# Kernel optimization log

Hardware: AMD Instinct MI355X
Metric: run time of the kernel (lower is better)

## Reference

```python
import jax, jax.numpy as jnp
import numpy as np

N_EMBD = 1024
N_HEAD = 16
B, T = 4, 2048

def setup_inputs() -> dict:
    key = jax.random.key(0)
    ks = jax.random.split(key, 5)
    s_attn = 1.0 / np.sqrt(N_EMBD)
    s_proj = 1.0 / np.sqrt(N_EMBD)
    return {
        "x": jax.random.normal(ks[0], (B, T, N_EMBD), dtype=jnp.float32),
        "w_attn": jax.random.uniform(ks[1], (N_EMBD, 3 * N_EMBD), jnp.float32, -s_attn, s_attn),
        "b_attn": jax.random.uniform(ks[2], (3 * N_EMBD,), jnp.float32, -s_attn, s_attn),
        "w_proj": jax.random.uniform(ks[3], (N_EMBD, N_EMBD), jnp.float32, -s_proj, s_proj),
        "b_proj": jax.random.uniform(ks[4], (N_EMBD,), jnp.float32, -s_proj, s_proj),
    }

def reference(x, w_attn, b_attn, w_proj, b_proj):
    Bx, Tx, C = x.shape
    hd = C // N_HEAD  # head dim
    qkv = x @ w_attn + b_attn                       # [B,T,3C]
    q, k, v = jnp.split(qkv, 3, axis=-1)
    # [B,T,C] -> [B,H,T,hd]
    def heads(t):
        return t.reshape(Bx, Tx, N_HEAD, hd).transpose(0, 2, 1, 3)
    q, k, v = heads(q), heads(k), heads(v)
    att = jnp.einsum('bhqd,bhkd->bhqk', q, k) * (1.0 / np.sqrt(hd))
    causal = jnp.tril(jnp.ones((Tx, Tx), dtype=bool))
    att = jnp.where(causal, att, -jnp.inf)
    att = jax.nn.softmax(att, axis=-1)
    y = jnp.einsum('bhqk,bhkd->bhqd', att, v)       # [B,H,T,hd]
    y = y.transpose(0, 2, 1, 3).reshape(Bx, Tx, C)
    return y @ w_proj + b_proj
```

## Files before the change

### kernel.cpp

```cpp
#include <hip/hip_runtime.h>
#include <cstdint>

typedef unsigned short u16;
typedef short s16x8 __attribute__((ext_vector_type(8)));
typedef short s16x4 __attribute__((ext_vector_type(4)));
typedef float f32x4 __attribute__((ext_vector_type(4)));
typedef float f32x16 __attribute__((ext_vector_type(16)));

#define B_   4
#define T_   2048
#define C_   1024
#define H_   16
#define HD_  64
#define M_   8192
#define N3_  3072

#define QSCALE 0.18033688011112042f

__device__ inline u16 f2b(float f) {
  union { float f; uint32_t u; } v; v.f = f;
  uint32_t u = v.u;
  return (u16)((u + 0x7FFFu + ((u >> 16) & 1u)) >> 16);
}

__device__ inline uint32_t cvtpk(float lo, float hi) {
  uint32_t r;
  asm("v_cvt_pk_bf16_f32 %0, %1, %2" : "=v"(r) : "v"(lo), "v"(hi));
  return r;
}

__device__ inline void gload_lds16(const void* g, void* l) {
  __builtin_amdgcn_global_load_lds(
      (const __attribute__((address_space(1))) void*)g,
      (__attribute__((address_space(3))) void*)l, 16, 0, 0);
}

__global__ __launch_bounds__(256) void cvt_f32_bf16(
    const float* __restrict__ in, u16* __restrict__ out, int n) {
  int i = (blockIdx.x * 256 + threadIdx.x) * 8;
  if (i >= n) return;
  float4 a = *(const float4*)(in + i);
  float4 b = *(const float4*)(in + i + 4);
  s16x8 r;
  r[0] = (short)f2b(a.x); r[1] = (short)f2b(a.y);
  r[2] = (short)f2b(a.z); r[3] = (short)f2b(a.w);
  r[4] = (short)f2b(b.x); r[5] = (short)f2b(b.y);
  r[6] = (short)f2b(b.z); r[7] = (short)f2b(b.w);
  *(s16x8*)(out + i) = r;
}

__global__ __launch_bounds__(256) void cvt_transpose(
    const float* __restrict__ W, u16* __restrict__ WT, int K, int N) {
  __shared__ u16 tile[64][65];
  int n0 = blockIdx.x * 64, k0 = blockIdx.y * 64;
  int j = threadIdx.x & 63, i0 = threadIdx.x >> 6;
#pragma unroll
  for (int i = i0; i < 64; i += 4)
    tile[i][j] = f2b(W[(size_t)(k0 + i) * N + n0 + j]);
  __syncthreads();
#pragma unroll
  for (int i = i0; i < 64; i += 4)
    WT[(size_t)(n0 + i) * K + k0 + j] = tile[j][i];
}

template <int MODE>
__global__ __launch_bounds__(256, 4) void gemm_bt(
    const u16* __restrict__ A, const u16* __restrict__ Bt,
    const float* __restrict__ bias, float* __restrict__ outf,
    u16* __restrict__ qo, u16* __restrict__ ko, u16* __restrict__ vo,
    int M, int N, int K) {
  __shared__ u16 As[128 * 64];
  __shared__ u16 Bs[128 * 64];

  int nwg = gridDim.x;
  int bid0 = blockIdx.x;
  int bid = (bid0 & 7) * (nwg >> 3) + (bid0 >> 3);
  int nbn = N >> 7;
  int bm = bid / nbn, bn = bid % nbn;
  int m0 = bm * 128, n0 = bn * 128;
  int tid = threadIdx.x;
  int lane = tid & 63, w = tid >> 6;
  int wm = (w >> 1) * 64, wn = (w & 1) * 64;
  int l15 = lane & 15, g = lane >> 4;

  f32x4 acc[4][4] = {};

  for (int kb = 0; kb < K; kb += 64) {
    __syncthreads();
#pragma unroll
    for (int p = 0; p < 4; ++p) {
      int idx = p * 256 + tid;
      int row = idx >> 3, pc = idx & 7;
      int sc = (pc ^ (row & 7)) * 8;
      gload_lds16(A  + (size_t)(m0 + row) * K + kb + sc, &As[idx * 8]);
      gload_lds16(Bt + (size_t)(n0 + row) * K + kb + sc, &Bs[idx * 8]);
    }
    __syncthreads();

#pragma unroll
    for (int ks = 0; ks < 2; ++ks) {
      int ck = ((g + 4 * ks) ^ (l15 & 7)) * 8;
      s16x8 af[4], bf[4];
#pragma unroll
      for (int mi = 0; mi < 4; ++mi)
        af[mi] = *(const s16x8*)&As[(wm + mi * 16 + l15) * 64 + ck];
#pragma unroll
      for (int ni = 0; ni < 4; ++ni)
        bf[ni] = *(const s16x8*)&Bs[(wn + ni * 16 + l15) * 64 + ck];
#pragma unroll
      for (int mi = 0; mi < 4; ++mi)
#pragma unroll
        for (int ni = 0; ni < 4; ++ni)
          acc[mi][ni] = __builtin_amdgcn_mfma_f32_16x16x32_bf16(
              af[mi], bf[ni], acc[mi][ni], 0, 0, 0);
    }
  }

#pragma unroll
  for (int mi = 0; mi < 4; ++mi)
#pragma unroll
    for (int ni = 0; ni < 4; ++ni) {
      int col = n0 + wn + ni * 16 + l15;
      float bv = bias[col];
      int row0 = m0 + wm + mi * 16 + g * 4;
      if (MODE == 0) {
#pragma unroll
        for (int r = 0; r < 4; ++r)
          outf[(size_t)(row0 + r) * N + col] = acc[mi][ni][r] + bv;
      } else {
        int which = col >> 10, hc = col & 1023;
        int h = hc >> 6, d = hc & 63;
        int b = row0 >> 11, t0 = row0 & 2047;
        if (which == 2) {
          s16x4 pv;
#pragma unroll
          for (int r = 0; r < 4; ++r) pv[r] = (short)f2b(acc[mi][ni][r] + bv);
          *(s16x4*)(vo + ((size_t)((b * 16 + h) * 64 + d)) * 2048 + t0) = pv;
        } else {
          u16* dst = (which == 0) ? qo : ko;
          float sc2 = (which == 0) ? QSCALE : 1.0f;
#pragma unroll
          for (int r = 0; r < 4; ++r)
            dst[(((size_t)(b * 16 + h)) * 2048 + (t0 + r)) * 64 + d] =
                f2b((acc[mi][ni][r] + bv) * sc2);
        }
      }
    }
}

__global__ __launch_bounds__(256, 3) void attn_fwd(
    const u16* __restrict__ Q, const u16* __restrict__ Kg,
    const u16* __restrict__ Vt, u16* __restrict__ Y) {
  __shared__ u16 Ks[64 * 64];
  __shared__ u16 Vs[64 * 64];

  int bid = blockIdx.x;
  int bh = bid & 63;
  int qb = 15 - (bid >> 6);
  int tid = threadIdx.x, lane = tid & 63, w = tid >> 6;
  int l31 = lane & 31, half = lane >> 5;

  const u16* Qh = Q  + (size_t)bh * T_ * HD_;
  const u16* Kh = Kg + (size_t)bh * T_ * HD_;
  const u16* Vh = Vt + (size_t)bh * HD_ * T_;

  int q0 = qb * 128;
  int qw = q0 + w * 32;
  int qrow = qw + l31;

  s16x8 qa[4];
#pragma unroll
  for (int kst = 0; kst < 4; ++kst)
    qa[kst] = *(const s16x8*)(Qh + (size_t)qrow * HD_ + kst * 16 + half * 8);

  f32x16 oacc[2] = {};
  float m = -3.0e30f, l = 0.f;

  int sr = tid >> 3, sc = tid & 7;
  int wswz = (sr & 7) << 4;
  int rswz = (l31 & 7) << 4;
  char* KsB = (char*)Ks;
  char* VsB = (char*)Vs;

  s16x8 kr0 = *(const s16x8*)(Kh + (size_t)sr * HD_ + sc * 8);
  s16x8 kr1 = *(const s16x8*)(Kh + (size_t)(sr + 32) * HD_ + sc * 8);
  s16x8 vr0 = *(const s16x8*)(Vh + (size_t)sr * T_ + sc * 8);
  s16x8 vr1 = *(const s16x8*)(Vh + (size_t)(sr + 32) * T_ + sc * 8);

  int ntile = 2 * qb + 2;
  for (int kt = 0; kt < ntile; ++kt) {
    int kvb = kt * 64;
    __syncthreads();
    *(s16x8*)(KsB + sr * 128 + ((sc * 16) ^ wswz))        = kr0;
    *(s16x8*)(KsB + (sr + 32) * 128 + ((sc * 16) ^ wswz)) = kr1;
    *(s16x8*)(VsB + sr * 128 + ((sc * 16) ^ wswz))        = vr0;
    *(s16x8*)(VsB + (sr + 32) * 128 + ((sc * 16) ^ wswz)) = vr1;
    __syncthreads();

    {
      int kvn = (kt + 1 < ntile) ? (kt + 1) * 64 : 0;
      kr0 = *(const s16x8*)(Kh + (size_t)(kvn + sr) * HD_ + sc * 8);
      kr1 = *(const s16x8*)(Kh + (size_t)(kvn + sr + 32) * HD_ + sc * 8);
      vr0 = *(const s16x8*)(Vh + (size_t)sr * T_ + kvn + sc * 8);
      vr1 = *(const s16x8*)(Vh + (size_t)(sr + 32) * T_ + kvn + sc * 8);
    }

    if (kvb > qw + 31) continue;

    f32x16 s0 = {}, s1 = {};
    __builtin_amdgcn_s_setprio(1);
#pragma unroll
    for (int kst = 0; kst < 4; ++kst) {
      s16x8 kb0 = *(const s16x8*)(KsB +
          (((l31) * 128 + kst * 32 + half * 16) ^ rswz));
      s0 = __builtin_amdgcn_mfma_f32_32x32x16_bf16(kb0, qa[kst], s0, 0, 0, 0);
      s16x8 kb1 = *(const s16x8*)(KsB +
          (((32 + l31) * 128 + kst * 32 + half * 16) ^ rswz));
      s1 = __builtin_amdgcn_mfma_f32_32x32x16_bf16(kb1, qa[kst], s1, 0, 0, 0);
    }
    __builtin_amdgcn_s_setprio(0);

    if (kvb + 63 > qw) {
#pragma unroll
      for (int r = 0; r < 16; ++r) {
        int kv0 = kvb + (r & 3) + 8 * (r >> 2) + 4 * half;
        if (kv0 > qrow) s0[r] = -1e30f;
        if (kv0 + 32 > qrow) s1[r] = -1e30f;
      }
    }

    float a0 = fmaxf(fmaxf(s0[0], s0[1]), fmaxf(s0[2], s0[3]));
    float a1 = fmaxf(fmaxf(s0[4], s0[5]), fmaxf(s0[6], s0[7]));
    float a2 = fmaxf(fmaxf(s0[8], s0[9]), fmaxf(s0[10], s0[11]));
    float a3 = fmaxf(fmaxf(s0[12], s0[13]), fmaxf(s0[14], s0[15]));
    float a4 = fmaxf(fmaxf(s1[0], s1[1]), fmaxf(s1[2], s1[3]));
    float a5 = fmaxf(fmaxf(s1[4], s1[5]), fmaxf(s1[6], s1[7]));
    float a6 = fmaxf(fmaxf(s1[8], s1[9]), fmaxf(s1[10], s1[11]));
    float a7 = fmaxf(fmaxf(s1[12], s1[13]), fmaxf(s1[14], s1[15]));
    float mx = fmaxf(fmaxf(fmaxf(a0, a1), fmaxf(a2, a3)),
                     fmaxf(fmaxf(a4, a5), fmaxf(a6, a7)));
    mx = fmaxf(mx, __shfl_xor(mx, 32, 64));

    if (!__all(mx <= m + 8.0f)) {
      float mn = fmaxf(m, mx);
      float alpha = __builtin_amdgcn_exp2f(m - mn);
      m = mn;
      l *= alpha;
#pragma unroll
      for (int i = 0; i < 16; ++i) { oacc[0][i] *= alpha; oacc[1][i] *= alpha; }
    }

    float rs = 0.f;
#pragma unroll
    for (int r = 0; r < 16; ++r) {
      float p0 = __builtin_amdgcn_exp2f(s0[r] - m);
      float p1 = __builtin_amdgcn_exp2f(s1[r] - m);
      s0[r] = p0; s1[r] = p1;
      rs += p0 + p1;
    }
    rs += __shfl_xor(rs, 32, 64);
    l += rs;

    s16x8 pb[4];
#pragma unroll
    for (int ks4 = 0; ks4 < 4; ++ks4) {
      const f32x16& sv = (ks4 < 2) ? s0 : s1;
      const int R = (ks4 & 1) * 8;
      uint32_t A0 = cvtpk(sv[R + 0], sv[R + 1]);
      uint32_t A1 = cvtpk(sv[R + 2], sv[R + 3]);
      uint32_t B0 = cvtpk(sv[R + 4], sv[R + 5]);
      uint32_t B1 = cvtpk(sv[R + 6], sv[R + 7]);
      uint32_t r0 = (uint32_t)__shfl_xor((int)(half ? A0 : B0), 32, 64);
      uint32_t r1 = (uint32_t)__shfl_xor((int)(half ? A1 : B1), 32, 64);
      union { uint32_t u[4]; s16x8 v; } pk_;
      pk_.u[0] = half ? r0 : A0;
      pk_.u[1] = half ? r1 : A1;
      pk_.u[2] = half ? B0 : r0;
      pk_.u[3] = half ? B1 : r1;
      pb[ks4] = pk_.v;
    }

    __builtin_amdgcn_s_setprio(1);
#pragma unroll
    for (int hb = 0; hb < 2; ++hb)
#pragma unroll
      for (int ks4 = 0; ks4 < 4; ++ks4) {
        s16x8 va = *(const s16x8*)(VsB +
            (((hb * 32 + l31) * 128 + ks4 * 32 + half * 16) ^ rswz));
        oacc[hb] = __builtin_amdgcn_mfma_f32_32x32x16_bf16(va, pb[ks4],
                                                           oacc[hb], 0, 0, 0);
      }
    __builtin_amdgcn_s_setprio(0);
  }

  int b = bh >> 4, h = bh & 15;
  float inv = 1.0f / l;
  u16* yrow = Y + ((size_t)b * T_ + qrow) * C_ + h * 64;
#pragma unroll
  for (int hb = 0; hb < 2; ++hb)
#pragma unroll
    for (int rg = 0; rg < 4; ++rg) {
      union { uint32_t u[2]; s16x4 v; } o;
      o.u[0] = cvtpk(oacc[hb][rg * 4 + 0] * inv, oacc[hb][rg * 4 + 1] * inv);
      o.u[1] = cvtpk(oacc[hb][rg * 4 + 2] * inv, oacc[hb][rg * 4 + 3] * inv);
      *(s16x4*)(yrow + hb * 32 + rg * 8 + half * 4) = o.v;
    }
}

extern "C" void kernel_launch(void* const* d_in, const int* in_sizes, int n_in,
                              void* d_out, int out_size, void* d_ws, size_t ws_size,
                              hipStream_t stream) {
  const float* x      = (const float*)d_in[0];
  const float* w_attn = (const float*)d_in[1];
  const float* b_attn = (const float*)d_in[2];
  const float* w_proj = (const float*)d_in[3];
  const float* b_proj = (const float*)d_in[4];
  float* out = (float*)d_out;

  u16* ws  = (u16*)d_ws;
  u16* xb  = ws;
  u16* wat = xb  + (size_t)M_ * C_;
  u16* wpt = wat + (size_t)N3_ * C_;
  u16* q   = wpt + (size_t)C_ * C_;
  u16* k   = q   + (size_t)M_ * C_;
  u16* v   = k   + (size_t)M_ * C_;
  u16* ya  = xb;

  cvt_f32_bf16<<<dim3((M_ * C_) / (256 * 8)), dim3(256), 0, stream>>>(x, xb, M_ * C_);
  cvt_transpose<<<dim3(N3_ / 64, C_ / 64), dim3(256), 0, stream>>>(w_attn, wat, C_, N3_);
  cvt_transpose<<<dim3(C_ / 64, C_ / 64), dim3(256), 0, stream>>>(w_proj, wpt, C_, C_);

  gemm_bt<1><<<dim3((M_ / 128) * (N3_ / 128)), dim3(256), 0, stream>>>(
      xb, wat, b_attn, nullptr, q, k, v, M_, N3_, C_);

  attn_fwd<<<dim3(64 * 16), dim3(256), 0, stream>>>(q, k, v, ya);

  gemm_bt<0><<<dim3((M_ / 128) * (C_ / 128)), dim3(256), 0, stream>>>(
      ya, wpt, b_proj, out, nullptr, nullptr, nullptr, M_, C_, C_);
}
```

Measured before the change: 166.5 us.

## Add 256x256 eight-wave ping-pong GEMM for QKV projection

Introduces a new gemm8p kernel with 256x256 tiles, 512 threads and double-buffered LDS. It interleaves global-to-LDS staging with MFMA quadrants under explicit barriers, waitcnts and setprio, and uses it for the QKV projection in place of the 128x128 gemm_bt. The aim is more data reuse per tile and better overlap of memory loads with matrix math. In exchange it uses 128KB of LDS per block and relies on hand-placed synchronization that is fragile and could stall if the waitcnt counts are wrong.

```diff
diff --git a/kernel.cpp b/kernel.cpp
--- a/kernel.cpp
+++ b/kernel.cpp
@@ -61,6 +61,160 @@
 #pragma unroll
   for (int i = i0; i < 64; i += 4)
     WT[(size_t)(n0 + i) * K + k0 + j] = tile[j][i];
+}
+
+template <int MODE>
+__global__ __launch_bounds__(512, 2) void gemm8p(
+    const u16* __restrict__ A, const u16* __restrict__ Bt,
+    const float* __restrict__ bias, float* __restrict__ outf,
+    u16* __restrict__ qo, u16* __restrict__ ko, u16* __restrict__ vo,
+    int M, int N, int K) {
+  __shared__ u16 As[2][2][128 * 64];
+  __shared__ u16 Bs[2][2][128 * 64];
+
+  int nwg = gridDim.x;
+  int bid0 = blockIdx.x;
+  int bid = (bid0 & 7) * (nwg >> 3) + (bid0 >> 3);
+  int nbn = N >> 8;
+  int bm = bid / nbn, bn = bid % nbn;
+  int m0 = bm * 256, n0 = bn * 256;
+  int tid = threadIdx.x, lane = tid & 63, w = tid >> 6;
+  int l15 = lane & 15, g = lane >> 4;
+  int Ah = w >> 2;
+  int Bh = (w & 3) >> 1;
+  int bno = (w & 1) * 64;
+  int nt = K >> 6;
+  int ck0 = (g ^ (l15 & 7)) * 8;
+  int ck1 = ((4 + g) ^ (l15 & 7)) * 8;
+
+  f32x4 acc[8][4] = {};
+  s16x8 af[4][2], bf0[2][2], bf1[2][2];
+
+#define BAR() asm volatile("s_barrier" ::: "memory")
+#define WAITL0() do { asm volatile("s_waitcnt lgkmcnt(0)" ::: "memory"); \
+  __builtin_amdgcn_sched_barrier(0); } while (0)
+#define STAGE_A8(bb, uh, kt) do { \
+  _Pragma("unroll") for (int ld = 0; ld < 2; ++ld) { \
+    int slot = ld * 512 + tid, row = slot >> 3, pc = slot & 7; \
+    int sc = (pc ^ (row & 7)) * 8; \
+    gload_lds16(A + (size_t)(m0 + (uh) * 128 + row) * K + (kt) * 64 + sc, \
+                &As[bb][uh][slot * 8]); \
+  } } while (0)
+#define STAGE_B8(bb, uh, kt) do { \
+  _Pragma("unroll") for (int ld = 0; ld < 2; ++ld) { \
+    int slot = ld * 512 + tid, row = slot >> 3, pc = slot & 7; \
+    int sc = (pc ^ (row & 7)) * 8; \
+    gload_lds16(Bt + (size_t)(n0 + (uh) * 128 + row) * K + (kt) * 64 + sc, \
+                &Bs[bb][uh][slot * 8]); \
+  } } while (0)
+#define LDA8(bb, mq) do { \
+  _Pragma("unroll") for (int mi = 0; mi < 4; ++mi) { \
+    int rw = ((mq) * 64 + mi * 16 + l15) * 64; \
+    af[mi][0] = *(const s16x8*)&As[bb][Ah][rw + ck0]; \
+    af[mi][1] = *(const s16x8*)&As[bb][Ah][rw + ck1]; \
+  } } while (0)
+#define LDB8(bb, nq, bfr) do { \
+  _Pragma("unroll") for (int ni = 0; ni < 2; ++ni) { \
+    int rw = (bno + (nq) * 32 + ni * 16 + l15) * 64; \
+    bfr[ni][0] = *(const s16x8*)&Bs[bb][Bh][rw + ck0]; \
+    bfr[ni][1] = *(const s16x8*)&Bs[bb][Bh][rw + ck1]; \
+  } } while (0)
+#define QUAD8(mq, nq, bfr) do { \
+  __builtin_amdgcn_s_setprio(1); \
+  _Pragma("unroll") for (int mi = 0; mi < 4; ++mi) \
+  _Pragma("unroll") for (int ni = 0; ni < 2; ++ni) \
+  _Pragma("unroll") for (int ks = 0; ks < 2; ++ks) \
+    acc[(mq) * 4 + mi][(nq) * 2 + ni] = \
+        __builtin_amdgcn_mfma_f32_16x16x32_bf16( \
+            af[mi][ks], bfr[ni][ks], acc[(mq) * 4 + mi][(nq) * 2 + ni], \
+            0, 0, 0); \
+  __builtin_amdgcn_s_setprio(0); \
+} while (0)
+
+  STAGE_B8(0, 0, 0); STAGE_B8(0, 1, 0);
+  STAGE_A8(0, 0, 0); STAGE_A8(0, 1, 0);
+  STAGE_B8(1, 0, 1); STAGE_B8(1, 1, 1);
+  asm volatile("s_waitcnt vmcnt(4)" ::: "memory");
+  BAR();
+
+  for (int t = 0; t < nt; t += 2) {
+    int t1 = t + 1;
+    int t2 = (t + 2 < nt) ? t + 2 : 0;
+    int t3 = (t + 3 < nt) ? t + 3 : 1;
+    LDA8(0, 0); LDB8(0, 0, bf0);
+    STAGE_A8(1, 0, t1);
+    asm volatile("s_waitcnt lgkmcnt(8)" ::: "memory");
+    BAR(); WAITL0();
+    QUAD8(0, 0, bf0); BAR();
+    LDB8(0, 1, bf1);
+    STAGE_A8(1, 1, t1);
+    BAR(); WAITL0();
+    QUAD8(0, 1, bf1); BAR();
+    LDA8(0, 1);
+    STAGE_B8(0, 0, t2);
+    BAR(); WAITL0();
+    QUAD8(1, 1, bf1); BAR();
+    STAGE_B8(0, 1, t2);
+    asm volatile("s_waitcnt vmcnt(4)" ::: "memory");
+    BAR();
+    QUAD8(1, 0, bf0); BAR();
+    LDA8(1, 0); LDB8(1, 0, bf0);
+    STAGE_A8(0, 0, t2);
+    asm volatile("s_waitcnt lgkmcnt(8)" ::: "memory");
+    BAR(); WAITL0();
+    QUAD8(0, 0, bf0); BAR();
+    LDB8(1, 1, bf1);
+    STAGE_A8(0, 1, t2);
+    BAR(); WAITL0();
+    QUAD8(0, 1, bf1); BAR();
+    LDA8(1, 1);
+    STAGE_B8(1, 0, t3);
+    BAR(); WAITL0();
+    QUAD8(1, 1, bf1); BAR();
+    STAGE_B8(1, 1, t3);
+    asm volatile("s_waitcnt vmcnt(4)" ::: "memory");
+    BAR();
+    QUAD8(1, 0, bf0); BAR();
+  }
+#undef BAR
+#undef WAITL0
+#undef STAGE_A8
+#undef STAGE_B8
+#undef LDA8
+#undef LDB8
+#undef QUAD8
+
+  int which = (MODE == 1) ? (n0 >> 10) : 0;
+#pragma unroll
+  for (int mf = 0; mf < 8; ++mf)
+#pragma unroll
+    for (int na = 0; na < 4; ++na) {
+      int col = n0 + (w & 3) * 64 + na * 16 + l15;
+      float bv = bias[col];
+      int row0 = m0 + (w >> 2) * 128 + mf * 16 + g * 4;
+      if (MODE == 0) {
+#pragma unroll
+        for (int r = 0; r < 4; ++r)
+          outf[(size_t)(row0 + r) * N + col] = acc[mf][na][r] + bv;
+      } else {
+        int hc = col & 1023;
+        int h = hc >> 6, d = hc & 63;
+        int b = row0 >> 11, t0 = row0 & 2047;
+        if (which == 2) {
+          s16x4 pv;
+#pragma unroll
+          for (int r = 0; r < 4; ++r) pv[r] = (short)f2b(acc[mf][na][r] + bv);
+          *(s16x4*)(vo + ((size_t)((b * 16 + h) * 64 + d)) * 2048 + t0) = pv;
+        } else {
+          u16* dst = (which == 0) ? qo : ko;
+          float sc2 = (which == 0) ? QSCALE : 1.0f;
+#pragma unroll
+          for (int r = 0; r < 4; ++r)
+            dst[(((size_t)(b * 16 + h)) * 2048 + (t0 + r)) * 64 + d] =
+                f2b((acc[mf][na][r] + bv) * sc2);
+        }
+      }
+    }
 }
 
 template <int MODE>
@@ -330,7 +484,7 @@
   cvt_transpose<<<dim3(N3_ / 64, C_ / 64), dim3(256), 0, stream>>>(w_attn, wat, C_, N3_);
   cvt_transpose<<<dim3(C_ / 64, C_ / 64), dim3(256), 0, stream>>>(w_proj, wpt, C_, C_);
 
-  gemm_bt<1><<<dim3((M_ / 128) * (N3_ / 128)), dim3(256), 0, stream>>>(
+  gemm8p<1><<<dim3((M_ / 256) * (N3_ / 256)), dim3(512), 0, stream>>>(
       xb, wat, b_attn, nullptr, q, k, v, M_, N3_, C_);
 
   attn_fwd<<<dim3(64 * 16), dim3(256), 0, stream>>>(q, k, v, ya);
```

New measurement: 173.0 us. 1.04x slower.

## Fuse fp32-to-bf16 conversion of x into QKV GEMM A-tile loading

Applied to the files above, without the earlier changes.

Removes the separate kernel that converted x to bf16. The QKV GEMM now reads fp32 A tiles straight into registers, one k-block ahead, and converts them with v_cvt_pk_bf16_f32 before writing them to LDS with the same swizzle. This drops one kernel launch and a full write plus re-read of the bf16 copy of x. In exchange, each QKV block moves twice as many A bytes (fp32) and is re-read across the 24 column tiles. It also uses more registers and replaces async LDS loads for A with synchronous register staging.

```diff
diff --git a/kernel.cpp b/kernel.cpp
--- a/kernel.cpp
+++ b/kernel.cpp
@@ -35,20 +35,6 @@
       (__attribute__((address_space(3))) void*)l, 16, 0, 0);
 }
 
-__global__ __launch_bounds__(256) void cvt_f32_bf16(
-    const float* __restrict__ in, u16* __restrict__ out, int n) {
-  int i = (blockIdx.x * 256 + threadIdx.x) * 8;
-  if (i >= n) return;
-  float4 a = *(const float4*)(in + i);
-  float4 b = *(const float4*)(in + i + 4);
-  s16x8 r;
-  r[0] = (short)f2b(a.x); r[1] = (short)f2b(a.y);
-  r[2] = (short)f2b(a.z); r[3] = (short)f2b(a.w);
-  r[4] = (short)f2b(b.x); r[5] = (short)f2b(b.y);
-  r[6] = (short)f2b(b.z); r[7] = (short)f2b(b.w);
-  *(s16x8*)(out + i) = r;
-}
-
 __global__ __launch_bounds__(256) void cvt_transpose(
     const float* __restrict__ W, u16* __restrict__ WT, int K, int N) {
   __shared__ u16 tile[64][65];
@@ -63,14 +49,16 @@
     WT[(size_t)(n0 + i) * K + k0 + j] = tile[j][i];
 }
 
-template <int MODE>
+template <int MODE, int AF32>
 __global__ __launch_bounds__(256, 4) void gemm_bt(
-    const u16* __restrict__ A, const u16* __restrict__ Bt,
+    const void* __restrict__ Araw, const u16* __restrict__ Bt,
     const float* __restrict__ bias, float* __restrict__ outf,
     u16* __restrict__ qo, u16* __restrict__ ko, u16* __restrict__ vo,
     int M, int N, int K) {
   __shared__ u16 As[128 * 64];
   __shared__ u16 Bs[128 * 64];
+  const u16*   A16 = (const u16*)Araw;
+  const float* A32 = (const float*)Araw;
 
   int nwg = gridDim.x;
   int bid0 = blockIdx.x;
@@ -85,17 +73,52 @@
 
   f32x4 acc[4][4] = {};
 
+  int tr = tid >> 4;
+  int tc = tid & 15;
+  const float* Afp = AF32 ? (A32 + (size_t)(m0 + tr) * K + tc * 4) : nullptr;
+  int aslot = ((tc >> 1) ^ (tr & 7)) * 8 + (tid & 1) * 4;
+  f32x4 fa[8];
+  if (AF32) {
+#pragma unroll
+    for (int p = 0; p < 8; ++p)
+      fa[p] = *(const f32x4*)(Afp + (size_t)p * 16 * K);
+  }
+
   for (int kb = 0; kb < K; kb += 64) {
     __syncthreads();
-#pragma unroll
-    for (int p = 0; p < 4; ++p) {
-      int idx = p * 256 + tid;
-      int row = idx >> 3, pc = idx & 7;
-      int sc = (pc ^ (row & 7)) * 8;
-      gload_lds16(A  + (size_t)(m0 + row) * K + kb + sc, &As[idx * 8]);
-      gload_lds16(Bt + (size_t)(n0 + row) * K + kb + sc, &Bs[idx * 8]);
+    if (AF32) {
+#pragma unroll
+      for (int p = 0; p < 8; ++p) {
+        uint32_t d0 = cvtpk(fa[p][0], fa[p][1]);
+        uint32_t d1 = cvtpk(fa[p][2], fa[p][3]);
+        uint2 dw; dw.x = d0; dw.y = d1;
+        *(uint2*)&As[(p * 16 + tr) * 64 + aslot] = dw;
+      }
+#pragma unroll
+      for (int p = 0; p < 4; ++p) {
+        int idx = p * 256 + tid;
+        int row = idx >> 3, pc = idx & 7;
+        int sc = (pc ^ (row & 7)) * 8;
+        gload_lds16(Bt + (size_t)(n0 + row) * K + kb + sc, &Bs[idx * 8]);
+      }
+    } else {
+#pragma unroll
+      for (int p = 0; p < 4; ++p) {
+        int idx = p * 256 + tid;
+        int row = idx >> 3, pc = idx & 7;
+        int sc = (pc ^ (row & 7)) * 8;
+        gload_lds16(A16 + (size_t)(m0 + row) * K + kb + sc, &As[idx * 8]);
+        gload_lds16(Bt  + (size_t)(n0 + row) * K + kb + sc, &Bs[idx * 8]);
+      }
     }
     __syncthreads();
+
+    if (AF32) {
+      int kn = (kb + 64 < K) ? kb + 64 : 0;
+#pragma unroll
+      for (int p = 0; p < 8; ++p)
+        fa[p] = *(const f32x4*)(Afp + (size_t)p * 16 * K + kn);
+    }
 
 #pragma unroll
     for (int ks = 0; ks < 2; ++ks) {
@@ -318,23 +341,21 @@
   float* out = (float*)d_out;
 
   u16* ws  = (u16*)d_ws;
-  u16* xb  = ws;
-  u16* wat = xb  + (size_t)M_ * C_;
+  u16* ya  = ws;
+  u16* wat = ya  + (size_t)M_ * C_;
   u16* wpt = wat + (size_t)N3_ * C_;
   u16* q   = wpt + (size_t)C_ * C_;
   u16* k   = q   + (size_t)M_ * C_;
   u16* v   = k   + (size_t)M_ * C_;
-  u16* ya  = xb;
-
-  cvt_f32_bf16<<<dim3((M_ * C_) / (256 * 8)), dim3(256), 0, stream>>>(x, xb, M_ * C_);
+
   cvt_transpose<<<dim3(N3_ / 64, C_ / 64), dim3(256), 0, stream>>>(w_attn, wat, C_, N3_);
   cvt_transpose<<<dim3(C_ / 64, C_ / 64), dim3(256), 0, stream>>>(w_proj, wpt, C_, C_);
 
-  gemm_bt<1><<<dim3((M_ / 128) * (N3_ / 128)), dim3(256), 0, stream>>>(
-      xb, wat, b_attn, nullptr, q, k, v, M_, N3_, C_);
+  gemm_bt<1, 1><<<dim3((M_ / 128) * (N3_ / 128)), dim3(256), 0, stream>>>(
+      x, wat, b_attn, nullptr, q, k, v, M_, N3_, C_);
 
   attn_fwd<<<dim3(64 * 16), dim3(256), 0, stream>>>(q, k, v, ya);
 
-  gemm_bt<0><<<dim3((M_ / 128) * (C_ / 128)), dim3(256), 0, stream>>>(
+  gemm_bt<0, 0><<<dim3((M_ / 128) * (C_ / 128)), dim3(256), 0, stream>>>(
       ya, wpt, b_proj, out, nullptr, nullptr, nullptr, M_, C_, C_);
 }
```

After: 165.6 us. Within noise of the previous version (-0.5%).

## Double per-warp query rows in attention to reuse K/V tiles across two blocks

Applied to the files above, without the earlier changes.

Each warp now processes two 32-row query blocks (256 queries per workgroup instead of 128), so every K/V fragment read from LDS feeds two MFMAs, and each K/V tile is loaded once per 256 queries. The grid halves to 512 workgroups and launch bounds drop to 2 waves-per-SIMD occupancy to fit the doubled accumulators and score registers. The trade-off is lower occupancy, coarser causal-block granularity with more masked waste, and fewer workgroups to balance across CUs.

```diff
diff --git a/kernel.cpp b/kernel.cpp
--- a/kernel.cpp
+++ b/kernel.cpp
@@ -148,7 +148,7 @@
     }
 }
 
-__global__ __launch_bounds__(256, 3) void attn_fwd(
+__global__ __launch_bounds__(256, 2) void attn_fwd(
     const u16* __restrict__ Q, const u16* __restrict__ Kg,
     const u16* __restrict__ Vt, u16* __restrict__ Y) {
   __shared__ u16 Ks[64 * 64];
@@ -156,7 +156,7 @@
 
   int bid = blockIdx.x;
   int bh = bid & 63;
-  int qb = 15 - (bid >> 6);
+  int qb = 7 - (bid >> 6);
   int tid = threadIdx.x, lane = tid & 63, w = tid >> 6;
   int l31 = lane & 31, half = lane >> 5;
 
@@ -164,17 +164,20 @@
   const u16* Kh = Kg + (size_t)bh * T_ * HD_;
   const u16* Vh = Vt + (size_t)bh * HD_ * T_;
 
-  int q0 = qb * 128;
-  int qw = q0 + w * 32;
-  int qrow = qw + l31;
-
-  s16x8 qa[4];
-#pragma unroll
-  for (int kst = 0; kst < 4; ++kst)
-    qa[kst] = *(const s16x8*)(Qh + (size_t)qrow * HD_ + kst * 16 + half * 8);
-
-  f32x16 oacc[2] = {};
-  float m = -3.0e30f, l = 0.f;
+  int q0 = qb * 256;
+  int qw = q0 + w * 64;
+  int qrA = qw + l31;
+  int qrB = qw + 32 + l31;
+
+  s16x8 qaA[4], qaB[4];
+#pragma unroll
+  for (int kst = 0; kst < 4; ++kst) {
+    qaA[kst] = *(const s16x8*)(Qh + (size_t)qrA * HD_ + kst * 16 + half * 8);
+    qaB[kst] = *(const s16x8*)(Qh + (size_t)qrB * HD_ + kst * 16 + half * 8);
+  }
+
+  f32x16 oA0 = {}, oA1 = {}, oB0 = {}, oB1 = {};
+  float mA = -3.0e30f, lA = 0.f, mB = -3.0e30f, lB = 0.f;
 
   int sr = tid >> 3, sc = tid & 7;
   int wswz = (sr & 7) << 4;
@@ -187,7 +190,7 @@
   s16x8 vr0 = *(const s16x8*)(Vh + (size_t)sr * T_ + sc * 8);
   s16x8 vr1 = *(const s16x8*)(Vh + (size_t)(sr + 32) * T_ + sc * 8);
 
-  int ntile = 2 * qb + 2;
+  int ntile = 4 * qb + 4;
   for (int kt = 0; kt < ntile; ++kt) {
     int kvb = kt * 64;
     __syncthreads();
@@ -205,18 +208,20 @@
       vr1 = *(const s16x8*)(Vh + (size_t)(sr + 32) * T_ + kvn + sc * 8);
     }
 
-    if (kvb > qw + 31) continue;
-
-    f32x16 s0 = {}, s1 = {};
+    if (kvb > qw + 63) continue;
+
+    f32x16 sA0 = {}, sA1 = {}, sB0 = {}, sB1 = {};
     __builtin_amdgcn_s_setprio(1);
 #pragma unroll
     for (int kst = 0; kst < 4; ++kst) {
       s16x8 kb0 = *(const s16x8*)(KsB +
-          (((l31) * 128 + kst * 32 + half * 16) ^ rswz));
-      s0 = __builtin_amdgcn_mfma_f32_32x32x16_bf16(kb0, qa[kst], s0, 0, 0, 0);
+          ((l31 * 128 + kst * 32 + half * 16) ^ rswz));
+      sA0 = __builtin_amdgcn_mfma_f32_32x32x16_bf16(kb0, qaA[kst], sA0, 0, 0, 0);
+      sB0 = __builtin_amdgcn_mfma_f32_32x32x16_bf16(kb0, qaB[kst], sB0, 0, 0, 0);
       s16x8 kb1 = *(const s16x8*)(KsB +
           (((32 + l31) * 128 + kst * 32 + half * 16) ^ rswz));
-      s1 = __builtin_amdgcn_mfma_f32_32x32x16_bf16(kb1, qa[kst], s1, 0, 0, 0);
+      sA1 = __builtin_amdgcn_mfma_f32_32x32x16_bf16(kb1, qaA[kst], sA1, 0, 0, 0);
+      sB1 = __builtin_amdgcn_mfma_f32_32x32x16_bf16(kb1, qaB[kst], sB1, 0, 0, 0);
     }
     __builtin_amdgcn_s_setprio(0);
 
@@ -224,87 +229,133 @@
 #pragma unroll
       for (int r = 0; r < 16; ++r) {
         int kv0 = kvb + (r & 3) + 8 * (r >> 2) + 4 * half;
-        if (kv0 > qrow) s0[r] = -1e30f;
-        if (kv0 + 32 > qrow) s1[r] = -1e30f;
+        if (kv0 > qrA)      sA0[r] = -1e30f;
+        if (kv0 + 32 > qrA) sA1[r] = -1e30f;
+        if (kv0 > qrB)      sB0[r] = -1e30f;
+        if (kv0 + 32 > qrB) sB1[r] = -1e30f;
       }
     }
 
-    float a0 = fmaxf(fmaxf(s0[0], s0[1]), fmaxf(s0[2], s0[3]));
-    float a1 = fmaxf(fmaxf(s0[4], s0[5]), fmaxf(s0[6], s0[7]));
-    float a2 = fmaxf(fmaxf(s0[8], s0[9]), fmaxf(s0[10], s0[11]));
-    float a3 = fmaxf(fmaxf(s0[12], s0[13]), fmaxf(s0[14], s0[15]));
-    float a4 = fmaxf(fmaxf(s1[0], s1[1]), fmaxf(s1[2], s1[3]));
-    float a5 = fmaxf(fmaxf(s1[4], s1[5]), fmaxf(s1[6], s1[7]));
-    float a6 = fmaxf(fmaxf(s1[8], s1[9]), fmaxf(s1[10], s1[11]));
-    float a7 = fmaxf(fmaxf(s1[12], s1[13]), fmaxf(s1[14], s1[15]));
-    float mx = fmaxf(fmaxf(fmaxf(a0, a1), fmaxf(a2, a3)),
-                     fmaxf(fmaxf(a4, a5), fmaxf(a6, a7)));
-    mx = fmaxf(mx, __shfl_xor(mx, 32, 64));
-
-    if (!__all(mx <= m + 8.0f)) {
-      float mn = fmaxf(m, mx);
-      float alpha = __builtin_amdgcn_exp2f(m - mn);
-      m = mn;
-      l *= alpha;
-#pragma unroll
-      for (int i = 0; i < 16; ++i) { oacc[0][i] *= alpha; oacc[1][i] *= alpha; }
-    }
-
-    float rs = 0.f;
+    float mxA, mxB;
+    {
+      float a0 = fmaxf(fmaxf(sA0[0], sA0[1]), fmaxf(sA0[2], sA0[3]));
+      float a1 = fmaxf(fmaxf(sA0[4], sA0[5]), fmaxf(sA0[6], sA0[7]));
+      float a2 = fmaxf(fmaxf(sA0[8], sA0[9]), fmaxf(sA0[10], sA0[11]));
+      float a3 = fmaxf(fmaxf(sA0[12], sA0[13]), fmaxf(sA0[14], sA0[15]));
+      float a4 = fmaxf(fmaxf(sA1[0], sA1[1]), fmaxf(sA1[2], sA1[3]));
+      float a5 = fmaxf(fmaxf(sA1[4], sA1[5]), fmaxf(sA1[6], sA1[7]));
+      float a6 = fmaxf(fmaxf(sA1[8], sA1[9]), fmaxf(sA1[10], sA1[11]));
+      float a7 = fmaxf(fmaxf(sA1[12], sA1[13]), fmaxf(sA1[14], sA1[15]));
+      mxA = fmaxf(fmaxf(fmaxf(a0, a1), fmaxf(a2, a3)),
+                  fmaxf(fmaxf(a4, a5), fmaxf(a6, a7)));
+      mxA = fmaxf(mxA, __shfl_xor(mxA, 32, 64));
+      float b0 = fmaxf(fmaxf(sB0[0], sB0[1]), fmaxf(sB0[2], sB0[3]));
+      float b1 = fmaxf(fmaxf(sB0[4], sB0[5]), fmaxf(sB0[6], sB0[7]));
+      float b2 = fmaxf(fmaxf(sB0[8], sB0[9]), fmaxf(sB0[10], sB0[11]));
+      float b3 = fmaxf(fmaxf(sB0[12], sB0[13]), fmaxf(sB0[14], sB0[15]));
+      float b4 = fmaxf(fmaxf(sB1[0], sB1[1]), fmaxf(sB1[2], sB1[3]));
+      float b5 = fmaxf(fmaxf(sB1[4], sB1[5]), fmaxf(sB1[6], sB1[7]));
+      float b6 = fmaxf(fmaxf(sB1[8], sB1[9]), fmaxf(sB1[10], sB1[11]));
+      float b7 = fmaxf(fmaxf(sB1[12], sB1[13]), fmaxf(sB1[14], sB1[15]));
+      mxB = fmaxf(fmaxf(fmaxf(b0, b1), fmaxf(b2, b3)),
+                  fmaxf(fmaxf(b4, b5), fmaxf(b6, b7)));
+      mxB = fmaxf(mxB, __shfl_xor(mxB, 32, 64));
+    }
+
+    if (!__all(mxA <= mA + 8.0f && mxB <= mB + 8.0f)) {
+      float mnA = fmaxf(mA, mxA), mnB = fmaxf(mB, mxB);
+      float aA = __builtin_amdgcn_exp2f(mA - mnA);
+      float aB = __builtin_amdgcn_exp2f(mB - mnB);
+      mA = mnA; mB = mnB;
+      lA *= aA; lB *= aB;
+#pragma unroll
+      for (int i = 0; i < 16; ++i) {
+        oA0[i] *= aA; oA1[i] *= aA;
+        oB0[i] *= aB; oB1[i] *= aB;
+      }
+    }
+
+    float rsA = 0.f, rsB = 0.f;
 #pragma unroll
     for (int r = 0; r < 16; ++r) {
-      float p0 = __builtin_amdgcn_exp2f(s0[r] - m);
-      float p1 = __builtin_amdgcn_exp2f(s1[r] - m);
-      s0[r] = p0; s1[r] = p1;
-      rs += p0 + p1;
-    }
-    rs += __shfl_xor(rs, 32, 64);
-    l += rs;
-
-    s16x8 pb[4];
+      float pa0 = __builtin_amdgcn_exp2f(sA0[r] - mA);
+      float pa1 = __builtin_amdgcn_exp2f(sA1[r] - mA);
+      float pb0 = __builtin_amdgcn_exp2f(sB0[r] - mB);
+      float pb1 = __builtin_amdgcn_exp2f(sB1[r] - mB);
+      sA0[r] = pa0; sA1[r] = pa1; sB0[r] = pb0; sB1[r] = pb1;
+      rsA += pa0 + pa1; rsB += pb0 + pb1;
+    }
+    rsA += __shfl_xor(rsA, 32, 64);
+    rsB += __shfl_xor(rsB, 32, 64);
+    lA += rsA; lB += rsB;
+
+    s16x8 pbA[4], pbB[4];
 #pragma unroll
     for (int ks4 = 0; ks4 < 4; ++ks4) {
-      const f32x16& sv = (ks4 < 2) ? s0 : s1;
+      const f32x16& svA = (ks4 < 2) ? sA0 : sA1;
+      const f32x16& svB = (ks4 < 2) ? sB0 : sB1;
       const int R = (ks4 & 1) * 8;
-      uint32_t A0 = cvtpk(sv[R + 0], sv[R + 1]);
-      uint32_t A1 = cvtpk(sv[R + 2], sv[R + 3]);
-      uint32_t B0 = cvtpk(sv[R + 4], sv[R + 5]);
-      uint32_t B1 = cvtpk(sv[R + 6], sv[R + 7]);
-      uint32_t r0 = (uint32_t)__shfl_xor((int)(half ? A0 : B0), 32, 64);
-      uint32_t r1 = (uint32_t)__shfl_xor((int)(half ? A1 : B1), 32, 64);
-      union { uint32_t u[4]; s16x8 v; } pk_;
-      pk_.u[0] = half ? r0 : A0;
-      pk_.u[1] = half ? r1 : A1;
-      pk_.u[2] = half ? B0 : r0;
-      pk_.u[3] = half ? B1 : r1;
-      pb[ks4] = pk_.v;
+      uint32_t Aa0 = cvtpk(svA[R + 0], svA[R + 1]);
+      uint32_t Aa1 = cvtpk(svA[R + 2], svA[R + 3]);
+      uint32_t Ab0 = cvtpk(svA[R + 4], svA[R + 5]);
+      uint32_t Ab1 = cvtpk(svA[R + 6], svA[R + 7]);
+      uint32_t ra0 = (uint32_t)__shfl_xor((int)(half ? Aa0 : Ab0), 32, 64);
+      uint32_t ra1 = (uint32_t)__shfl_xor((int)(half ? Aa1 : Ab1), 32, 64);
+      union { uint32_t u[4]; s16x8 v; } pkA;
+      pkA.u[0] = half ? ra0 : Aa0;
+      pkA.u[1] = half ? ra1 : Aa1;
+      pkA.u[2] = half ? Ab0 : ra0;
+      pkA.u[3] = half ? Ab1 : ra1;
+      pbA[ks4] = pkA.v;
+      uint32_t Ba0 = cvtpk(svB[R + 0], svB[R + 1]);
+      uint32_t Ba1 = cvtpk(svB[R + 2], svB[R + 3]);
+      uint32_t Bb0 = cvtpk(svB[R + 4], svB[R + 5]);
+      uint32_t Bb1 = cvtpk(svB[R + 6], svB[R + 7]);
+      uint32_t rb0 = (uint32_t)__shfl_xor((int)(half ? Ba0 : Bb0), 32, 64);
+      uint32_t rb1 = (uint32_t)__shfl_xor((int)(half ? Ba1 : Bb1), 32, 64);
+      union { uint32_t u[4]; s16x8 v; } pkB;
+      pkB.u[0] = half ? rb0 : Ba0;
+      pkB.u[1] = half ? rb1 : Ba1;
+      pkB.u[2] = half ? Bb0 : rb0;
+      pkB.u[3] = half ? Bb1 : rb1;
+      pbB[ks4] = pkB.v;
     }
 
     __builtin_amdgcn_s_setprio(1);
 #pragma unroll
-    for (int hb = 0; hb < 2; ++hb)
-#pragma unroll
-      for (int ks4 = 0; ks4 < 4; ++ks4) {
-        s16x8 va = *(const s16x8*)(VsB +
-            (((hb * 32 + l31) * 128 + ks4 * 32 + half * 16) ^ rswz));
-        oacc[hb] = __builtin_amdgcn_mfma_f32_32x32x16_bf16(va, pb[ks4],
-                                                           oacc[hb], 0, 0, 0);
-      }
+    for (int ks4 = 0; ks4 < 4; ++ks4) {
+      s16x8 va0 = *(const s16x8*)(VsB +
+          ((l31 * 128 + ks4 * 32 + half * 16) ^ rswz));
+      oA0 = __builtin_amdgcn_mfma_f32_32x32x16_bf16(va0, pbA[ks4], oA0, 0, 0, 0);
+      oB0 = __builtin_amdgcn_mfma_f32_32x32x16_bf16(va0, pbB[ks4], oB0, 0, 0, 0);
+      s16x8 va1 = *(const s16x8*)(VsB +
+          (((32 + l31) * 128 + ks4 * 32 + half * 16) ^ rswz));
+      oA1 = __builtin_amdgcn_mfma_f32_32x32x16_bf16(va1, pbA[ks4], oA1, 0, 0, 0);
+      oB1 = __builtin_amdgcn_mfma_f32_32x32x16_bf16(va1, pbB[ks4], oB1, 0, 0, 0);
+    }
     __builtin_amdgcn_s_setprio(0);
   }
 
   int b = bh >> 4, h = bh & 15;
-  float inv = 1.0f / l;
-  u16* yrow = Y + ((size_t)b * T_ + qrow) * C_ + h * 64;
-#pragma unroll
-  for (int hb = 0; hb < 2; ++hb)
-#pragma unroll
-    for (int rg = 0; rg < 4; ++rg) {
-      union { uint32_t u[2]; s16x4 v; } o;
-      o.u[0] = cvtpk(oacc[hb][rg * 4 + 0] * inv, oacc[hb][rg * 4 + 1] * inv);
-      o.u[1] = cvtpk(oacc[hb][rg * 4 + 2] * inv, oacc[hb][rg * 4 + 3] * inv);
-      *(s16x4*)(yrow + hb * 32 + rg * 8 + half * 4) = o.v;
-    }
+  float invA = 1.0f / lA, invB = 1.0f / lB;
+  u16* yrA = Y + ((size_t)b * T_ + qrA) * C_ + h * 64;
+  u16* yrB = Y + ((size_t)b * T_ + qrB) * C_ + h * 64;
+#pragma unroll
+  for (int rg = 0; rg < 4; ++rg) {
+    union { uint32_t u[2]; s16x4 v; } o;
+    o.u[0] = cvtpk(oA0[rg * 4 + 0] * invA, oA0[rg * 4 + 1] * invA);
+    o.u[1] = cvtpk(oA0[rg * 4 + 2] * invA, oA0[rg * 4 + 3] * invA);
+    *(s16x4*)(yrA + rg * 8 + half * 4) = o.v;
+    o.u[0] = cvtpk(oA1[rg * 4 + 0] * invA, oA1[rg * 4 + 1] * invA);
+    o.u[1] = cvtpk(oA1[rg * 4 + 2] * invA, oA1[rg * 4 + 3] * invA);
+    *(s16x4*)(yrA + 32 + rg * 8 + half * 4) = o.v;
+    o.u[0] = cvtpk(oB0[rg * 4 + 0] * invB, oB0[rg * 4 + 1] * invB);
+    o.u[1] = cvtpk(oB0[rg * 4 + 2] * invB, oB0[rg * 4 + 3] * invB);
+    *(s16x4*)(yrB + rg * 8 + half * 4) = o.v;
+    o.u[0] = cvtpk(oB1[rg * 4 + 0] * invB, oB1[rg * 4 + 1] * invB);
+    o.u[1] = cvtpk(oB1[rg * 4 + 2] * invB, oB1[rg * 4 + 3] * invB);
+    *(s16x4*)(yrB + 32 + rg * 8 + half * 4) = o.v;
+  }
 }
 
 extern "C" void kernel_launch(void* const* d_in, const int* in_sizes, int n_in,
@@ -333,7 +384,7 @@
   gemm_bt<1><<<dim3((M_ / 128) * (N3_ / 128)), dim3(256), 0, stream>>>(
       xb, wat, b_attn, nullptr, q, k, v, M_, N3_, C_);
 
-  attn_fwd<<<dim3(64 * 16), dim3(256), 0, stream>>>(q, k, v, ya);
+  attn_fwd<<<dim3(64 * 8), dim3(256), 0, stream>>>(q, k, v, ya);
 
   gemm_bt<0><<<dim3((M_ / 128) * (C_ / 128)), dim3(256), 0, stream>>>(
       ya, wpt, b_proj, out, nullptr, nullptr, nullptr, M_, C_, C_);
```

After: 184.4 us. 1.11x slower.
